# Kernel optimization log

Measured on AMD Instinct MI355X. Metric: run time of the kernel, lower is better.

## Reference

```python
import jax, jax.numpy as jnp
import numpy as np

B_, L_, OBS = 16, 1024, 64
H, NB, NST, DC, EXP = 256, 4, 16, 4, 2
DIN = EXP * H          # 512
DTR = (H + 15) // 16   # dt_rank = 16


def setup_inputs() -> dict:
    key = jax.random.key(0)
    ks = jax.random.split(key, 12)
    s = 0.02
    A_log = jnp.tile(jnp.log(jnp.arange(1, NST + 1, dtype=jnp.float32)), (NB, DIN, 1))
    return {
        "x": jax.random.normal(ks[0], (B_, L_, OBS), jnp.float32),
        "proj_w": jax.random.normal(ks[1], (H, OBS), jnp.float32) * s,
        "proj_b": jnp.zeros((H,), jnp.float32),
        "in_proj_w": jax.random.normal(ks[2], (NB, 2 * DIN, H), jnp.float32) * s,
        "conv_w": jax.random.normal(ks[3], (NB, DIN, DC), jnp.float32) * s,
        "conv_b": jnp.zeros((NB, DIN), jnp.float32),
        "x_proj_w": jax.random.normal(ks[4], (NB, DTR + 2 * NST, DIN), jnp.float32) * s,
        "dt_proj_w": jax.random.normal(ks[5], (NB, DIN, DTR), jnp.float32) * s,
        "dt_proj_b": jax.random.normal(ks[6], (NB, DIN), jnp.float32) * 0.1 - 3.0,
        "A_log": A_log,
        "D_skip": jnp.ones((NB, DIN), jnp.float32),
        "out_proj_w": jax.random.normal(ks[7], (NB, H, DIN), jnp.float32) * s,
        "head_w": jax.random.normal(ks[8], (1, H), jnp.float32) * s,
        "head_b": jnp.zeros((1,), jnp.float32),
    }


def _mamba(x, ipw, cw, cb, xpw, dpw, dpb, Alog, Dsk, opw):
    # x: [B, L, H]
    Bb, L, _ = x.shape
    xz = jnp.einsum('blh,eh->ble', x, ipw)           # [B,L,2*DIN]
    xin, z = jnp.split(xz, 2, axis=-1)
    # causal depthwise conv1d
    xc = jnp.transpose(xin, (0, 2, 1))               # [B,DIN,L]
    xc = jax.lax.conv_general_dilated(
        xc, cw[:, None, :], (1,), [(DC - 1, 0)],
        dimension_numbers=('NCH', 'OIH', 'NCH'), feature_group_count=DIN)
    u = jax.nn.silu(jnp.transpose(xc + cb[None, :, None], (0, 2, 1)))  # [B,L,DIN]
    # input-dependent dt, B, C
    proj = jnp.einsum('bld,ed->ble', u, xpw)         # [B,L,DTR+2*NST]
    dtl, Bc, Cc = jnp.split(proj, [DTR, DTR + NST], axis=-1)
    dt = jax.nn.softplus(jnp.einsum('blr,dr->bld', dtl, dpw) + dpb)     # [B,L,DIN]
    A = -jnp.exp(Alog)                               # [DIN,NST]

    def step(h, t):
        dt_t, B_t, C_t, u_t = t                      # [B,DIN],[B,NST],[B,NST],[B,DIN]
        h = jnp.exp(dt_t[:, :, None] * A) * h + (dt_t * u_t)[:, :, None] * B_t[:, None, :]
        return h, jnp.einsum('bdn,bn->bd', h, C_t)

    seq = (jnp.moveaxis(dt, 1, 0), jnp.moveaxis(Bc, 1, 0),
           jnp.moveaxis(Cc, 1, 0), jnp.moveaxis(u, 1, 0))
    h0 = jnp.zeros((Bb, DIN, NST), x.dtype)
    _, ys = jax.lax.scan(step, h0, seq)              # [L,B,DIN]
    y = jnp.moveaxis(ys, 0, 1) + Dsk * u
    y = y * jax.nn.silu(z)
    return jnp.einsum('bld,hd->blh', y, opw)


def reference(x, proj_w, proj_b, in_proj_w, conv_w, conv_b, x_proj_w,
              dt_proj_w, dt_proj_b, A_log, D_skip, out_proj_w, head_w, head_b):
    h = jnp.einsum('blo,ho->blh', x, proj_w) + proj_b
    for i in range(NB):
        h = _mamba(h, in_proj_w[i], conv_w[i], conv_b[i], x_proj_w[i],
                   dt_proj_w[i], dt_proj_b[i], A_log[i], D_skip[i], out_proj_w[i])
    v = jnp.einsum('bh,oh->bo', h[:, -1, :], head_w) + head_b  # [B,1]
    return v.squeeze(-1)
```

## Files before the change

kernel.cpp:

```cpp
#include <hip/hip_runtime.h>
#include <cstddef>

#define Bb 16
#define Ll 1024
#define OBS 64
#define Hh 256
#define NBLK 4
#define NST 16
#define DCV 4
#define DIN 512
#define DTR 16
#define NC 32
#define CL (Ll / NC)

typedef short short8 __attribute__((ext_vector_type(8)));
typedef float f32x4 __attribute__((ext_vector_type(4)));

static const size_t OFF_H0   = 0;
static const size_t OFF_H1   = OFF_H0 + (size_t)Bb * Ll * Hh;
static const size_t OFF_XIN  = OFF_H1 + (size_t)Bb * Ll * Hh;
static const size_t OFF_Z    = OFF_XIN + (size_t)Bb * Ll * DIN;
static const size_t OFF_U    = OFF_Z   + (size_t)Bb * Ll * DIN;
static const size_t OFF_PROJ = OFF_U   + (size_t)Bb * Ll * DIN;
static const size_t OFF_HST  = OFF_PROJ + (size_t)Bb * Ll * 48;
static const size_t OFF_WC   = OFF_HST + (size_t)Bb * NC * NST * DIN;
static const size_t WPW_HI  = 0;
static const size_t WPW_LO  = 16384;
static const size_t WIPW_HI = 32768;
static const size_t WIPW_LO = WIPW_HI + 1048576;
static const size_t WOPW_HI = WIPW_LO + 1048576;
static const size_t WOPW_LO = WOPW_HI + 524288;

__device__ inline unsigned short f32_to_bf16(float v) {
    unsigned int u = __float_as_uint(v);
    u += 0x7fffu + ((u >> 16) & 1u);
    return (unsigned short)(u >> 16);
}
__device__ inline float bf16_to_f32(unsigned short h) {
    return __uint_as_float((unsigned int)h << 16);
}
__device__ inline float softplusf(float s) {
    return fmaxf(s, 0.f) + log1pf(__expf(-fabsf(s)));
}

__global__ __launch_bounds__(256) void convert_w_kernel(
    const float* __restrict__ w,
    unsigned short* __restrict__ hi,
    unsigned short* __restrict__ lo, int n4)
{
    int i = blockIdx.x * 256 + threadIdx.x;
    if (i >= n4) return;
    float4 v4 = ((const float4*)w)[i];
    float vv[4] = {v4.x, v4.y, v4.z, v4.w};
#pragma unroll
    for (int e = 0; e < 4; ++e) {
        unsigned short hb = f32_to_bf16(vv[e]);
        float res = vv[e] - bf16_to_f32(hb);
        hi[i * 4 + e] = hb;
        lo[i * 4 + e] = f32_to_bf16(res);
    }
}

template <int BM, int WR>
__global__ __launch_bounds__(256) void gemm_mfma3(
    const float* __restrict__ A, int lda,
    const unsigned short* __restrict__ Whi,
    const unsigned short* __restrict__ Wlo,
    const float* __restrict__ bias,
    float* __restrict__ C0,
    float* __restrict__ C1,
    int N, int K, int splitN)
{
    constexpr int WC_ = 4 / WR;
    constexpr int MI = (BM / WR) / 16;
    constexpr int NJ = (128 / WC_) / 16;
    constexpr int ASLOT = BM * 4 / 256;

    __shared__ unsigned short AsH[BM * 32], AsL[BM * 32];
    __shared__ unsigned short BsH[128 * 32], BsL[128 * 32];

    const int tid  = threadIdx.x;
    const int lane = tid & 63;
    const int w    = tid >> 6;
    const int wr   = w / WC_;
    const int wc   = w % WC_;
    const int m0   = blockIdx.y * BM;
    const int n0   = blockIdx.x * 128;

    f32x4 acc[MI][NJ] = {};

    for (int k0 = 0; k0 < K; k0 += 32) {
#pragma unroll
        for (int sI = 0; sI < ASLOT; ++sI) {
            int s = tid + sI * 256;
            int row = s >> 2, kb = s & 3;
            const float* ap = A + (size_t)(m0 + row) * lda + k0 + kb * 8;
            float4 v0 = *(const float4*)ap;
            float4 v1 = *(const float4*)(ap + 4);
            float vv[8] = {v0.x, v0.y, v0.z, v0.w, v1.x, v1.y, v1.z, v1.w};
            short8 h8, l8;
#pragma unroll
            for (int e = 0; e < 8; ++e) {
                unsigned short hb = f32_to_bf16(vv[e]);
                float res = vv[e] - bf16_to_f32(hb);
                h8[e] = (short)hb;
                l8[e] = (short)f32_to_bf16(res);
            }
            *(short8*)&AsH[s * 8] = h8;
            *(short8*)&AsL[s * 8] = l8;
        }
#pragma unroll
        for (int sI = 0; sI < 2; ++sI) {
            int s = tid + sI * 256;
            int row = s >> 2, kb = s & 3;
            size_t off = (size_t)(n0 + row) * K + k0 + kb * 8;
            *(short8*)&BsH[s * 8] = *(const short8*)(Whi + off);
            *(short8*)&BsL[s * 8] = *(const short8*)(Wlo + off);
        }
        __syncthreads();

        const int rr = lane & 15;
        const int kq = lane >> 4;
        short8 ah[MI], al[MI];
#pragma unroll
        for (int i = 0; i < MI; ++i) {
            int row = wr * (BM / WR) + i * 16 + rr;
            ah[i] = *(const short8*)&AsH[row * 32 + kq * 8];
            al[i] = *(const short8*)&AsL[row * 32 + kq * 8];
        }
#pragma unroll
        for (int j = 0; j < NJ; ++j) {
            int col = wc * (128 / WC_) + j * 16 + rr;
            short8 bh = *(const short8*)&BsH[col * 32 + kq * 8];
            short8 bl = *(const short8*)&BsL[col * 32 + kq * 8];
#pragma unroll
            for (int i = 0; i < MI; ++i) {
                acc[i][j] = __builtin_amdgcn_mfma_f32_16x16x32_bf16(ah[i], bh, acc[i][j], 0, 0, 0);
                acc[i][j] = __builtin_amdgcn_mfma_f32_16x16x32_bf16(ah[i], bl, acc[i][j], 0, 0, 0);
                acc[i][j] = __builtin_amdgcn_mfma_f32_16x16x32_bf16(al[i], bh, acc[i][j], 0, 0, 0);
            }
        }
        __syncthreads();
    }

    const int rr = lane & 15;
    const int rq = lane >> 4;
#pragma unroll
    for (int i = 0; i < MI; ++i) {
#pragma unroll
        for (int j = 0; j < NJ; ++j) {
            int col = n0 + wc * (128 / WC_) + j * 16 + rr;
            float badd = bias ? bias[col] : 0.f;
#pragma unroll
            for (int r = 0; r < 4; ++r) {
                int row = m0 + wr * (BM / WR) + i * 16 + rq * 4 + r;
                float v = acc[i][j][r] + badd;
                if (col < splitN)
                    C0[(size_t)row * splitN + col] = v;
                else
                    C1[(size_t)row * (N - splitN) + (col - splitN)] = v;
            }
        }
    }
}

template <int ACT>
__global__ __launch_bounds__(256) void gemm_nt(
    const float* __restrict__ A, int lda,
    const float* __restrict__ W,
    const float* __restrict__ bias,
    float* __restrict__ C0, float* __restrict__ C1,
    int M, int N, int K, int splitN)
{
    __shared__ float As[16][68];
    __shared__ float Ws[16][68];

    const int tid = threadIdx.x;
    const int m0 = blockIdx.y * 64;
    const int n0 = blockIdx.x * 64;
    const int tx = tid & 15;
    const int ty = tid >> 4;
    const int r  = tid >> 2;
    const int kv = (tid & 3) * 4;

    float acc[4][4] = {};

    for (int k0 = 0; k0 < K; k0 += 16) {
        float4 a4;
        {
            const float* ap = A + (size_t)(m0 + r) * lda + (k0 + kv);
            a4 = *(const float4*)ap;
        }
        float4 w4 = make_float4(0.f, 0.f, 0.f, 0.f);
        if (n0 + r < N) {
            const float* wp = W + (size_t)(n0 + r) * K + (k0 + kv);
            w4 = *(const float4*)wp;
        }
        __syncthreads();
        As[kv + 0][r] = a4.x; As[kv + 1][r] = a4.y;
        As[kv + 2][r] = a4.z; As[kv + 3][r] = a4.w;
        Ws[kv + 0][r] = w4.x; Ws[kv + 1][r] = w4.y;
        Ws[kv + 2][r] = w4.z; Ws[kv + 3][r] = w4.w;
        __syncthreads();
#pragma unroll
        for (int kk = 0; kk < 16; ++kk) {
            float4 av = *(const float4*)&As[kk][ty * 4];
            float4 wv = *(const float4*)&Ws[kk][tx * 4];
            float am[4] = {av.x, av.y, av.z, av.w};
            float wn[4] = {wv.x, wv.y, wv.z, wv.w};
#pragma unroll
            for (int i = 0; i < 4; ++i)
#pragma unroll
                for (int j = 0; j < 4; ++j)
                    acc[i][j] += am[i] * wn[j];
        }
    }

#pragma unroll
    for (int i = 0; i < 4; ++i) {
        const int row = m0 + ty * 4 + i;
#pragma unroll
        for (int j = 0; j < 4; ++j) {
            const int col = n0 + tx * 4 + j;
            if (col >= N) continue;
            float v = acc[i][j];
            if (bias) v += bias[col];
            if (ACT == 1) v = softplusf(v);
            if (col < splitN)
                C0[(size_t)row * splitN + col] = v;
            else
                C1[(size_t)row * (N - splitN) + (col - splitN)] = v;
        }
    }
}

__global__ __launch_bounds__(256) void conv_silu_kernel(
    const float* __restrict__ xin,
    const float* __restrict__ cw,
    const float* __restrict__ cb,
    float* __restrict__ u, int total4)
{
    int i = blockIdx.x * 256 + threadIdx.x;
    if (i >= total4) return;
    int d4 = (i & (DIN / 4 - 1)) * 4;
    int bl = i >> 7;
    int l  = bl & (Ll - 1);

    float4 cb4 = *(const float4*)(cb + d4);
    float acc[4] = {cb4.x, cb4.y, cb4.z, cb4.w};
    float4 cw0 = *(const float4*)(cw + (d4 + 0) * 4);
    float4 cw1 = *(const float4*)(cw + (d4 + 1) * 4);
    float4 cw2 = *(const float4*)(cw + (d4 + 2) * 4);
    float4 cw3 = *(const float4*)(cw + (d4 + 3) * 4);
    const float* cwp[4] = {(const float*)&cw0, (const float*)&cw1,
                           (const float*)&cw2, (const float*)&cw3};
#pragma unroll
    for (int k = 0; k < DCV; ++k) {
        int ls = l - (DCV - 1) + k;
        if (ls >= 0) {
            float4 xv = *(const float4*)(xin + (size_t)(bl - (DCV - 1) + k) * DIN + d4);
            float xj[4] = {xv.x, xv.y, xv.z, xv.w};
#pragma unroll
            for (int j = 0; j < 4; ++j) acc[j] += xj[j] * cwp[j][k];
        }
    }
    float4 o;
    o.x = acc[0] / (1.f + __expf(-acc[0]));
    o.y = acc[1] / (1.f + __expf(-acc[1]));
    o.z = acc[2] / (1.f + __expf(-acc[2]));
    o.w = acc[3] / (1.f + __expf(-acc[3]));
    *(float4*)(u + (size_t)bl * DIN + d4) = o;
}

__global__ __launch_bounds__(256) void scan_chunk_reduce(
    const float* __restrict__ dt,
    const float* __restrict__ u,
    const float* __restrict__ proj,
    const float* __restrict__ Alog,
    float* __restrict__ P,
    float* __restrict__ F)
{
    const int tid  = threadIdx.x;
    const int lane = tid & 63;
    const int widx = blockIdx.x * 4 + (tid >> 6);
    const int ng = lane >> 5;
    const int dd = lane & 31;
    const int d32 = widx & 15;
    const int c   = (widx >> 4) & (NC - 1);
    const int b   = widx >> 9;
    const int d   = d32 * 32 + dd;
    const int nb  = ng * 8;

    float A[8];
#pragma unroll
    for (int j = 0; j < 8; ++j) A[j] = -__expf(Alog[d * NST + nb + j]);

    float h[8], p[8];
#pragma unroll
    for (int j = 0; j < 8; ++j) { h[j] = 0.f; p[j] = 1.f; }

    const int l0 = c * CL;
    for (int l = l0; l < l0 + CL; ++l) {
        size_t row = (size_t)b * Ll + l;
        float dtv = dt[row * DIN + d];
        float uv  = u[row * DIN + d];
        float du  = dtv * uv;
        const float* pr = proj + row * 48;
        float4 B0 = *(const float4*)(pr + DTR + nb);
        float4 B1 = *(const float4*)(pr + DTR + nb + 4);
        float Bn[8] = {B0.x, B0.y, B0.z, B0.w, B1.x, B1.y, B1.z, B1.w};
#pragma unroll
        for (int j = 0; j < 8; ++j) {
            float e = __expf(dtv * A[j]);
            h[j] = e * h[j] + du * Bn[j];
            p[j] *= e;
        }
    }

    size_t base = (((size_t)b * NC + c) * NST + nb) * DIN + d;
#pragma unroll
    for (int j = 0; j < 8; ++j) {
        P[base + (size_t)j * DIN] = p[j];
        F[base + (size_t)j * DIN] = h[j];
    }
}

__global__ __launch_bounds__(256) void scan_prefix(
    const float* __restrict__ P,
    const float* __restrict__ F,
    float* __restrict__ HST)
{
    int gid = blockIdx.x * 256 + threadIdx.x;
    int d = gid & (DIN - 1);
    int n = (gid >> 9) & (NST - 1);
    int b = gid >> 13;

    const size_t stride = (size_t)NST * DIN;
    size_t idx = (((size_t)b * NC + 0) * NST + n) * DIN + d;

    float pc = P[idx], fc = F[idx];
    float h = 0.f;
    for (int c = 0; c < NC; ++c) {
        float pn = 0.f, fn = 0.f;
        if (c + 1 < NC) {
            pn = P[idx + stride];
            fn = F[idx + stride];
        }
        HST[idx] = h;
        h = pc * h + fc;
        pc = pn; fc = fn;
        idx += stride;
    }
}

__global__ __launch_bounds__(256) void scan_rescan_gate(
    const float* __restrict__ dt,
    const float* __restrict__ u,
    const float* __restrict__ proj,
    const float* __restrict__ Alog,
    const float* __restrict__ Dsk,
    const float* __restrict__ z,
    const float* __restrict__ HST,
    float* __restrict__ g)
{
    const int tid  = threadIdx.x;
    const int lane = tid & 63;
    const int widx = blockIdx.x * 4 + (tid >> 6);
    const int ng = lane >> 5;
    const int dd = lane & 31;
    const int d32 = widx & 15;
    const int c   = (widx >> 4) & (NC - 1);
    const int b   = widx >> 9;
    const int d   = d32 * 32 + dd;
    const int nb  = ng * 8;

    float A[8];
#pragma unroll
    for (int j = 0; j < 8; ++j) A[j] = -__expf(Alog[d * NST + nb + j]);
    const float Dv = Dsk[d];

    float h[8];
    {
        size_t base = (((size_t)b * NC + c) * NST + nb) * DIN + d;
#pragma unroll
        for (int j = 0; j < 8; ++j) h[j] = HST[base + (size_t)j * DIN];
    }

    const int l0 = c * CL;
    for (int l = l0; l < l0 + CL; ++l) {
        size_t row = (size_t)b * Ll + l;
        float dtv = dt[row * DIN + d];
        float uv  = u[row * DIN + d];
        float du  = dtv * uv;
        const float* pr = proj + row * 48;
        float4 B0 = *(const float4*)(pr + DTR + nb);
        float4 B1 = *(const float4*)(pr + DTR + nb + 4);
        float4 C0 = *(const float4*)(pr + 2 * DTR + nb);
        float4 C1 = *(const float4*)(pr + 2 * DTR + nb + 4);
        float Bn[8] = {B0.x, B0.y, B0.z, B0.w, B1.x, B1.y, B1.z, B1.w};
        float Cn[8] = {C0.x, C0.y, C0.z, C0.w, C1.x, C1.y, C1.z, C1.w};
        float y = 0.f;
#pragma unroll
        for (int j = 0; j < 8; ++j) {
            float e = __expf(dtv * A[j]);
            h[j] = e * h[j] + du * Bn[j];
            y += h[j] * Cn[j];
        }
        y += __shfl_xor(y, 32);
        if (ng == 0) {
            float zv = z[row * DIN + d];
            float sig = zv / (1.f + __expf(-zv));
            g[row * DIN + d] = (y + Dv * uv) * sig;
        }
    }
}

__global__ void head_kernel(const float* __restrict__ h,
                            const float* __restrict__ hw,
                            const float* __restrict__ hb,
                            float* __restrict__ out)
{
    int b = blockIdx.x;
    int t = threadIdx.x;
    const float* row = h + ((size_t)b * Ll + (Ll - 1)) * Hh;
    float s = 0.f;
    for (int j = t; j < Hh; j += 64) s += row[j] * hw[j];
#pragma unroll
    for (int off = 32; off; off >>= 1) s += __shfl_down(s, off);
    if (t == 0) out[b] = s + hb[0];
}

extern "C" void kernel_launch(void* const* d_in, const int* in_sizes, int n_in,
                              void* d_out, int out_size, void* d_ws, size_t ws_size,
                              hipStream_t stream)
{
    const float* x    = (const float*)d_in[0];
    const float* pw   = (const float*)d_in[1];
    const float* pb   = (const float*)d_in[2];
    const float* ipw  = (const float*)d_in[3];
    const float* cw   = (const float*)d_in[4];
    const float* cb   = (const float*)d_in[5];
    const float* xpw  = (const float*)d_in[6];
    const float* dpw  = (const float*)d_in[7];
    const float* dpb  = (const float*)d_in[8];
    const float* Alog = (const float*)d_in[9];
    const float* Dsk  = (const float*)d_in[10];
    const float* opw  = (const float*)d_in[11];
    const float* hw   = (const float*)d_in[12];
    const float* hb   = (const float*)d_in[13];
    float* out = (float*)d_out;
    float* ws  = (float*)d_ws;

    float* h_buf[2] = { ws + OFF_H0, ws + OFF_H1 };
    float* xin  = ws + OFF_XIN;
    float* zb   = ws + OFF_Z;
    float* ub   = ws + OFF_U;
    float* prj  = ws + OFF_PROJ;
    float* hst  = ws + OFF_HST;
    float* dtb  = xin;
    unsigned short* wc = (unsigned short*)(ws + OFF_WC);

    const int M = Bb * Ll;

    convert_w_kernel<<<(Hh * OBS / 4 + 255) / 256, 256, 0, stream>>>(
        pw, wc + WPW_HI, wc + WPW_LO, Hh * OBS / 4);
    convert_w_kernel<<<(NBLK * 2 * DIN * Hh / 4 + 255) / 256, 256, 0, stream>>>(
        ipw, wc + WIPW_HI, wc + WIPW_LO, NBLK * 2 * DIN * Hh / 4);
    convert_w_kernel<<<(NBLK * Hh * DIN / 4 + 255) / 256, 256, 0, stream>>>(
        opw, wc + WOPW_HI, wc + WOPW_LO, NBLK * Hh * DIN / 4);

    gemm_mfma3<64, 1><<<dim3(Hh / 128, M / 64), 256, 0, stream>>>(
        x, OBS, wc + WPW_HI, wc + WPW_LO, pb, h_buf[0], nullptr, Hh, OBS, Hh);

    int cur = 0;
    for (int i = 0; i < NBLK; ++i) {
        const unsigned short* ipwh = wc + WIPW_HI + (size_t)i * 2 * DIN * Hh;
        const unsigned short* ipwl = wc + WIPW_LO + (size_t)i * 2 * DIN * Hh;
        const unsigned short* opwh = wc + WOPW_HI + (size_t)i * Hh * DIN;
        const unsigned short* opwl = wc + WOPW_LO + (size_t)i * Hh * DIN;
        const float* cw_i  = cw  + (size_t)i * DIN * DCV;
        const float* cb_i  = cb  + (size_t)i * DIN;
        const float* xpw_i = xpw + (size_t)i * 48 * DIN;
        const float* dpw_i = dpw + (size_t)i * DIN * DTR;
        const float* dpb_i = dpb + (size_t)i * DIN;
        const float* Al_i  = Alog + (size_t)i * DIN * NST;
        const float* Dk_i  = Dsk + (size_t)i * DIN;

        gemm_mfma3<128, 2><<<dim3(2 * DIN / 128, M / 128), 256, 0, stream>>>(
            h_buf[cur], Hh, ipwh, ipwl, nullptr, xin, zb, 2 * DIN, Hh, DIN);

        conv_silu_kernel<<<(M * DIN / 4) / 256, 256, 0, stream>>>(
            xin, cw_i, cb_i, ub, M * DIN / 4);

        gemm_nt<0><<<dim3(1, M / 64), 256, 0, stream>>>(
            ub, DIN, xpw_i, nullptr, prj, nullptr, M, 48, DIN, 48);

        gemm_nt<1><<<dim3(DIN / 64, M / 64), 256, 0, stream>>>(
            prj, 48, dpw_i, dpb_i, dtb, nullptr, M, DIN, DTR, DIN);

        float* Pbuf = h_buf[cur];
        float* Fbuf = h_buf[cur ^ 1];
        scan_chunk_reduce<<<(Bb * NC * DIN * 2) / 1024 * 4 / 4, 256, 0, stream>>>(
            dtb, ub, prj, Al_i, Pbuf, Fbuf);
        scan_prefix<<<(Bb * NST * DIN) / 256, 256, 0, stream>>>(
            Pbuf, Fbuf, hst);
        scan_rescan_gate<<<(Bb * NC * DIN * 2) / 1024 * 4 / 4, 256, 0, stream>>>(
            dtb, ub, prj, Al_i, Dk_i, zb, hst, ub);

        gemm_mfma3<64, 1><<<dim3(Hh / 128, M / 64), 256, 0, stream>>>(
            ub, DIN, opwh, opwl, nullptr, h_buf[cur ^ 1], nullptr, Hh, DIN, Hh);

        cur ^= 1;
    }

    head_kernel<<<Bb, 64, 0, stream>>>(h_buf[cur], hw, hb, out);
}
```

Baseline: 889.6 us.

## Store hidden state as split bf16 pairs and stage GEMM tiles via direct LDS loads

```diff
diff --git a/kernel.cpp b/kernel.cpp
--- a/kernel.cpp
+++ b/kernel.cpp
@@ -16,9 +16,10 @@
 typedef short short8 __attribute__((ext_vector_type(8)));
 typedef float f32x4 __attribute__((ext_vector_type(4)));
 
-static const size_t OFF_H0   = 0;
-static const size_t OFF_H1   = OFF_H0 + (size_t)Bb * Ll * Hh;
-static const size_t OFF_XIN  = OFF_H1 + (size_t)Bb * Ll * Hh;
+#define HSZ ((size_t)Bb * Ll * Hh)
+static const size_t OFF_P    = 0;
+static const size_t OFF_F    = HSZ;
+static const size_t OFF_XIN  = 2 * HSZ;
 static const size_t OFF_Z    = OFF_XIN + (size_t)Bb * Ll * DIN;
 static const size_t OFF_U    = OFF_Z   + (size_t)Bb * Ll * DIN;
 static const size_t OFF_PROJ = OFF_U   + (size_t)Bb * Ll * DIN;
@@ -42,6 +43,11 @@
 __device__ inline float softplusf(float s) {
     return fmaxf(s, 0.f) + log1pf(__expf(-fabsf(s)));
 }
+__device__ inline void gload16(const void* g, void* l) {
+    __builtin_amdgcn_global_load_lds(
+        (const __attribute__((address_space(1))) void*)g,
+        (__attribute__((address_space(3))) void*)l, 16, 0, 0);
+}
 
 __global__ __launch_bounds__(256) void convert_w_kernel(
     const float* __restrict__ w,
@@ -62,19 +68,19 @@
 }
 
 template <int BM, int WR>
-__global__ __launch_bounds__(256) void gemm_mfma3(
-    const float* __restrict__ A, int lda,
+__global__ __launch_bounds__(256) void gemm_bs(
+    const unsigned short* __restrict__ Ahi,
+    const unsigned short* __restrict__ Alo, int lda,
     const unsigned short* __restrict__ Whi,
     const unsigned short* __restrict__ Wlo,
     const float* __restrict__ bias,
-    float* __restrict__ C0,
-    float* __restrict__ C1,
-    int N, int K, int splitN)
+    float* __restrict__ C0, float* __restrict__ C1,
+    int nbx, int N, int K, int splitN)
 {
     constexpr int WC_ = 4 / WR;
     constexpr int MI = (BM / WR) / 16;
     constexpr int NJ = (128 / WC_) / 16;
-    constexpr int ASLOT = BM * 4 / 256;
+    constexpr int ASL = BM * 4 / 256;
 
     __shared__ unsigned short AsH[BM * 32], AsL[BM * 32];
     __shared__ unsigned short BsH[128 * 32], BsL[128 * 32];
@@ -84,38 +90,31 @@
     const int w    = tid >> 6;
     const int wr   = w / WC_;
     const int wc   = w % WC_;
-    const int m0   = blockIdx.y * BM;
-    const int n0   = blockIdx.x * 128;
+
+    const int swz = (blockIdx.x & 7) * (gridDim.x >> 3) + (blockIdx.x >> 3);
+    const int m0 = (swz / nbx) * BM;
+    const int n0 = (swz % nbx) * 128;
 
     f32x4 acc[MI][NJ] = {};
 
     for (int k0 = 0; k0 < K; k0 += 32) {
 #pragma unroll
-        for (int sI = 0; sI < ASLOT; ++sI) {
+        for (int sI = 0; sI < ASL; ++sI) {
             int s = tid + sI * 256;
             int row = s >> 2, kb = s & 3;
-            const float* ap = A + (size_t)(m0 + row) * lda + k0 + kb * 8;
-            float4 v0 = *(const float4*)ap;
-            float4 v1 = *(const float4*)(ap + 4);
-            float vv[8] = {v0.x, v0.y, v0.z, v0.w, v1.x, v1.y, v1.z, v1.w};
-            short8 h8, l8;
-#pragma unroll
-            for (int e = 0; e < 8; ++e) {
-                unsigned short hb = f32_to_bf16(vv[e]);
-                float res = vv[e] - bf16_to_f32(hb);
-                h8[e] = (short)hb;
-                l8[e] = (short)f32_to_bf16(res);
-            }
-            *(short8*)&AsH[s * 8] = h8;
-            *(short8*)&AsL[s * 8] = l8;
+            int kb2 = kb ^ ((row >> 1) & 3);
+            size_t go = (size_t)(m0 + row) * lda + k0 + kb2 * 8;
+            gload16(Ahi + go, &AsH[s * 8]);
+            gload16(Alo + go, &AsL[s * 8]);
         }
 #pragma unroll
         for (int sI = 0; sI < 2; ++sI) {
             int s = tid + sI * 256;
             int row = s >> 2, kb = s & 3;
-            size_t off = (size_t)(n0 + row) * K + k0 + kb * 8;
-            *(short8*)&BsH[s * 8] = *(const short8*)(Whi + off);
-            *(short8*)&BsL[s * 8] = *(const short8*)(Wlo + off);
+            int kb2 = kb ^ ((row >> 1) & 3);
+            size_t go = (size_t)(n0 + row) * K + k0 + kb2 * 8;
+            gload16(Whi + go, &BsH[s * 8]);
+            gload16(Wlo + go, &BsL[s * 8]);
         }
         __syncthreads();
 
@@ -125,14 +124,16 @@
 #pragma unroll
         for (int i = 0; i < MI; ++i) {
             int row = wr * (BM / WR) + i * 16 + rr;
-            ah[i] = *(const short8*)&AsH[row * 32 + kq * 8];
-            al[i] = *(const short8*)&AsL[row * 32 + kq * 8];
+            int off = row * 32 + (kq ^ ((row >> 1) & 3)) * 8;
+            ah[i] = *(const short8*)&AsH[off];
+            al[i] = *(const short8*)&AsL[off];
         }
 #pragma unroll
         for (int j = 0; j < NJ; ++j) {
             int col = wc * (128 / WC_) + j * 16 + rr;
-            short8 bh = *(const short8*)&BsH[col * 32 + kq * 8];
-            short8 bl = *(const short8*)&BsL[col * 32 + kq * 8];
+            int off = col * 32 + (kq ^ ((col >> 1) & 3)) * 8;
+            short8 bh = *(const short8*)&BsH[off];
+            short8 bl = *(const short8*)&BsL[off];
 #pragma unroll
             for (int i = 0; i < MI; ++i) {
                 acc[i][j] = __builtin_amdgcn_mfma_f32_16x16x32_bf16(ah[i], bh, acc[i][j], 0, 0, 0);
@@ -159,6 +160,122 @@
                     C0[(size_t)row * splitN + col] = v;
                 else
                     C1[(size_t)row * (N - splitN) + (col - splitN)] = v;
+            }
+        }
+    }
+}
+
+template <int BM, int WR, int OUT>
+__global__ __launch_bounds__(256) void gemm_mfma3(
+    const float* __restrict__ A, int lda,
+    const unsigned short* __restrict__ Whi,
+    const unsigned short* __restrict__ Wlo,
+    const float* __restrict__ bias,
+    float* __restrict__ C0, float* __restrict__ C1,
+    int nbx, int N, int K, int splitN)
+{
+    constexpr int WC_ = 4 / WR;
+    constexpr int MI = (BM / WR) / 16;
+    constexpr int NJ = (128 / WC_) / 16;
+    constexpr int ASL = BM * 4 / 256;
+
+    __shared__ unsigned short AsH[BM * 32], AsL[BM * 32];
+    __shared__ unsigned short BsH[128 * 32], BsL[128 * 32];
+
+    const int tid  = threadIdx.x;
+    const int lane = tid & 63;
+    const int w    = tid >> 6;
+    const int wr   = w / WC_;
+    const int wc   = w % WC_;
+
+    const int swz = (blockIdx.x & 7) * (gridDim.x >> 3) + (blockIdx.x >> 3);
+    const int m0 = (swz / nbx) * BM;
+    const int n0 = (swz % nbx) * 128;
+
+    f32x4 acc[MI][NJ] = {};
+
+    for (int k0 = 0; k0 < K; k0 += 32) {
+#pragma unroll
+        for (int sI = 0; sI < 2; ++sI) {
+            int s = tid + sI * 256;
+            int row = s >> 2, kb = s & 3;
+            int kb2 = kb ^ ((row >> 1) & 3);
+            size_t go = (size_t)(n0 + row) * K + k0 + kb2 * 8;
+            gload16(Whi + go, &BsH[s * 8]);
+            gload16(Wlo + go, &BsL[s * 8]);
+        }
+#pragma unroll
+        for (int sI = 0; sI < ASL; ++sI) {
+            int s = tid + sI * 256;
+            int row = s >> 2, kb = s & 3;
+            int kb2 = kb ^ ((row >> 1) & 3);
+            const float* ap = A + (size_t)(m0 + row) * lda + k0 + kb * 8;
+            float4 v0 = *(const float4*)ap;
+            float4 v1 = *(const float4*)(ap + 4);
+            float vv[8] = {v0.x, v0.y, v0.z, v0.w, v1.x, v1.y, v1.z, v1.w};
+            short8 h8, l8;
+#pragma unroll
+            for (int e = 0; e < 8; ++e) {
+                unsigned short hb = f32_to_bf16(vv[e]);
+                float res = vv[e] - bf16_to_f32(hb);
+                h8[e] = (short)hb;
+                l8[e] = (short)f32_to_bf16(res);
+            }
+            *(short8*)&AsH[row * 32 + kb2 * 8] = h8;
+            *(short8*)&AsL[row * 32 + kb2 * 8] = l8;
+        }
+        __syncthreads();
+
+        const int rr = lane & 15;
+        const int kq = lane >> 4;
+        short8 ah[MI], al[MI];
+#pragma unroll
+        for (int i = 0; i < MI; ++i) {
+            int row = wr * (BM / WR) + i * 16 + rr;
+            int off = row * 32 + (kq ^ ((row >> 1) & 3)) * 8;
+            ah[i] = *(const short8*)&AsH[off];
+            al[i] = *(const short8*)&AsL[off];
+        }
+#pragma unroll
+        for (int j = 0; j < NJ; ++j) {
+            int col = wc * (128 / WC_) + j * 16 + rr;
+            int off = col * 32 + (kq ^ ((col >> 1) & 3)) * 8;
+            short8 bh = *(const short8*)&BsH[off];
+            short8 bl = *(const short8*)&BsL[off];
+#pragma unroll
+            for (int i = 0; i < MI; ++i) {
+                acc[i][j] = __builtin_amdgcn_mfma_f32_16x16x32_bf16(ah[i], bh, acc[i][j], 0, 0, 0);
+                acc[i][j] = __builtin_amdgcn_mfma_f32_16x16x32_bf16(ah[i], bl, acc[i][j], 0, 0, 0);
+                acc[i][j] = __builtin_amdgcn_mfma_f32_16x16x32_bf16(al[i], bh, acc[i][j], 0, 0, 0);
+            }
+        }
+        __syncthreads();
+    }
+
+    const int rr = lane & 15;
+    const int rq = lane >> 4;
+    unsigned short* Hd = (unsigned short*)C0;
+    unsigned short* Ld = (unsigned short*)C1;
+#pragma unroll
+    for (int i = 0; i < MI; ++i) {
+#pragma unroll
+        for (int j = 0; j < NJ; ++j) {
+            int col = n0 + wc * (128 / WC_) + j * 16 + rr;
+            float badd = bias ? bias[col] : 0.f;
+#pragma unroll
+            for (int r = 0; r < 4; ++r) {
+                int row = m0 + wr * (BM / WR) + i * 16 + rq * 4 + r;
+                float v = acc[i][j][r] + badd;
+                if (OUT == 0) {
+                    if (col < splitN)
+                        C0[(size_t)row * splitN + col] = v;
+                    else
+                        C1[(size_t)row * (N - splitN) + (col - splitN)] = v;
+                } else {
+                    unsigned short hb = f32_to_bf16(v);
+                    Hd[(size_t)row * N + col] = hb;
+                    Ld[(size_t)row * N + col] = f32_to_bf16(v - bf16_to_f32(hb));
+                }
             }
         }
     }
@@ -415,16 +532,18 @@
     }
 }
 
-__global__ void head_kernel(const float* __restrict__ h,
+__global__ void head_kernel(const unsigned short* __restrict__ hhi,
+                            const unsigned short* __restrict__ hlo,
                             const float* __restrict__ hw,
                             const float* __restrict__ hb,
                             float* __restrict__ out)
 {
     int b = blockIdx.x;
     int t = threadIdx.x;
-    const float* row = h + ((size_t)b * Ll + (Ll - 1)) * Hh;
+    const size_t base = ((size_t)b * Ll + (Ll - 1)) * Hh;
     float s = 0.f;
-    for (int j = t; j < Hh; j += 64) s += row[j] * hw[j];
+    for (int j = t; j < Hh; j += 64)
+        s += (bf16_to_f32(hhi[base + j]) + bf16_to_f32(hlo[base + j])) * hw[j];
 #pragma unroll
     for (int off = 32; off; off >>= 1) s += __shfl_down(s, off);
     if (t == 0) out[b] = s + hb[0];
@@ -451,7 +570,11 @@
     float* out = (float*)d_out;
     float* ws  = (float*)d_ws;
 
-    float* h_buf[2] = { ws + OFF_H0, ws + OFF_H1 };
+    unsigned short* hs = (unsigned short*)ws;
+    unsigned short* h_hi[2] = { hs,           hs + 2 * HSZ };
+    unsigned short* h_lo[2] = { hs + HSZ,     hs + 3 * HSZ };
+    float* Pbuf = ws + OFF_P;
+    float* Fbuf = ws + OFF_F;
     float* xin  = ws + OFF_XIN;
     float* zb   = ws + OFF_Z;
     float* ub   = ws + OFF_U;
@@ -461,6 +584,7 @@
     unsigned short* wc = (unsigned short*)(ws + OFF_WC);
 
     const int M = Bb * Ll;
+    const int SCAN_BLOCKS = Bb * NC * (DIN / 32) / 4;
 
     convert_w_kernel<<<(Hh * OBS / 4 + 255) / 256, 256, 0, stream>>>(
         pw, wc + WPW_HI, wc + WPW_LO, Hh * OBS / 4);
@@ -469,8 +593,9 @@
     convert_w_kernel<<<(NBLK * Hh * DIN / 4 + 255) / 256, 256, 0, stream>>>(
         opw, wc + WOPW_HI, wc + WOPW_LO, NBLK * Hh * DIN / 4);
 
-    gemm_mfma3<64, 1><<<dim3(Hh / 128, M / 64), 256, 0, stream>>>(
-        x, OBS, wc + WPW_HI, wc + WPW_LO, pb, h_buf[0], nullptr, Hh, OBS, Hh);
+    gemm_mfma3<64, 1, 1><<<dim3((Hh / 128) * (M / 64)), 256, 0, stream>>>(
+        x, OBS, wc + WPW_HI, wc + WPW_LO, pb,
+        (float*)h_hi[0], (float*)h_lo[0], Hh / 128, Hh, OBS, Hh);
 
     int cur = 0;
     for (int i = 0; i < NBLK; ++i) {
@@ -486,8 +611,9 @@
         const float* Al_i  = Alog + (size_t)i * DIN * NST;
         const float* Dk_i  = Dsk + (size_t)i * DIN;
 
-        gemm_mfma3<128, 2><<<dim3(2 * DIN / 128, M / 128), 256, 0, stream>>>(
-            h_buf[cur], Hh, ipwh, ipwl, nullptr, xin, zb, 2 * DIN, Hh, DIN);
+        gemm_bs<128, 2><<<dim3((2 * DIN / 128) * (M / 128)), 256, 0, stream>>>(
+            h_hi[cur], h_lo[cur], Hh, ipwh, ipwl, nullptr,
+            xin, zb, 2 * DIN / 128, 2 * DIN, Hh, DIN);
 
         conv_silu_kernel<<<(M * DIN / 4) / 256, 256, 0, stream>>>(
             xin, cw_i, cb_i, ub, M * DIN / 4);
@@ -498,20 +624,19 @@
         gemm_nt<1><<<dim3(DIN / 64, M / 64), 256, 0, stream>>>(
             prj, 48, dpw_i, dpb_i, dtb, nullptr, M, DIN, DTR, DIN);
 
-        float* Pbuf = h_buf[cur];
-        float* Fbuf = h_buf[cur ^ 1];
-        scan_chunk_reduce<<<(Bb * NC * DIN * 2) / 1024 * 4 / 4, 256, 0, stream>>>(
+        scan_chunk_reduce<<<SCAN_BLOCKS, 256, 0, stream>>>(
             dtb, ub, prj, Al_i, Pbuf, Fbuf);
         scan_prefix<<<(Bb * NST * DIN) / 256, 256, 0, stream>>>(
             Pbuf, Fbuf, hst);
-        scan_rescan_gate<<<(Bb * NC * DIN * 2) / 1024 * 4 / 4, 256, 0, stream>>>(
+        scan_rescan_gate<<<SCAN_BLOCKS, 256, 0, stream>>>(
             dtb, ub, prj, Al_i, Dk_i, zb, hst, ub);
 
-        gemm_mfma3<64, 1><<<dim3(Hh / 128, M / 64), 256, 0, stream>>>(
-            ub, DIN, opwh, opwl, nullptr, h_buf[cur ^ 1], nullptr, Hh, DIN, Hh);
+        gemm_mfma3<64, 1, 1><<<dim3((Hh / 128) * (M / 64)), 256, 0, stream>>>(
+            ub, DIN, opwh, opwl, nullptr,
+            (float*)h_hi[cur ^ 1], (float*)h_lo[cur ^ 1], Hh / 128, Hh, DIN, Hh);
 
         cur ^= 1;
     }
 
-    head_kernel<<<Bb, 64, 0, stream>>>(h_buf[cur], hw, hb, out);
-}
+    head_kernel<<<Bb, 64, 0, stream>>>(h_hi[cur], h_lo[cur], hw, hb, out);
+}
```

Result: slower. 1.035 ms (+16.3%).
